# Performance work log

Hardware: AMD Instinct MI355X
Metric: run time of the kernel (lower is better)

The kernel has to match this reference:

```python
import jax, jax.numpy as jnp
import numpy as np

B, C, H, W = 8, 256, 48, 48
CK = 64  # C // k
WSCALE = 0.3 / np.sqrt(C)  # keep exp(QK^T) finite (original has no 1/sqrt(d) scaling)


def conv1x1(x, w, b):
    # x: (B,C,H,W), w: (O,C,1,1), b: (O,) -> (B,O,H,W)
    return jnp.einsum('bchw,oc->bohw', x, w[:, :, 0, 0]) + b[None, :, None, None]


def setup_inputs() -> dict:
    key = jax.random.key(0)
    ks = jax.random.split(key, 6)
    x = jax.random.normal(ks[0], (B, C, H, W), dtype=jnp.float32)
    qw = jax.random.normal(ks[1], (CK, C, 1, 1), dtype=jnp.float32) * WSCALE
    kw = jax.random.normal(ks[2], (CK, C, 1, 1), dtype=jnp.float32) * WSCALE
    vw = jax.random.normal(ks[3], (C, C, 1, 1), dtype=jnp.float32) * (1.0 / np.sqrt(C))
    gw = jax.random.normal(ks[4], (C, C, 1, 1), dtype=jnp.float32) * (1.0 / np.sqrt(C))
    zk = jnp.zeros((CK,), dtype=jnp.float32)
    zc = jnp.zeros((C,), dtype=jnp.float32)
    return {
        'x': x,
        'query_weight': qw, 'query_bias': zk,
        'key_weight': kw, 'key_bias': zk,
        'value_weight': vw, 'value_bias': zc,
        'gamma_weight': gw, 'gamma_bias': zc,
        'k': 4,
    }


def reference(x, query_weight, query_bias, key_weight, key_bias,
              value_weight, value_bias, gamma_weight, gamma_bias, k):
    b, c, h, w = x.shape
    n = h * w
    q = conv1x1(x, query_weight, query_bias).reshape(b, -1, n)   # (B,Ck,N)
    kk = conv1x1(x, key_weight, key_bias).reshape(b, -1, n)      # (B,Ck,N)
    # energy[b,i,j] = q_i . k_j  (queries on rows, no sqrt(d) scaling)
    energy = jnp.einsum('bci,bcj->bij', q, kk)                   # (B,N,N)
    energy = jnp.exp(energy)
    energy = energy / jnp.sum(energy, axis=2, keepdims=True)     # unnormalized-softmax over keys
    v = conv1x1(x, value_weight, value_bias).reshape(b, c, n)    # (B,C,N)
    # out[b,c,j] = sum_i v[b,c,i] * energy[b,i,j]  (faithful to torch.bmm(V, energy))
    out = jnp.einsum('bci,bij->bcj', v, energy).reshape(b, c, h, w)
    out = conv1x1(out, gamma_weight, gamma_bias)
    return out
```

## Files before the change

### kernel.cpp

```cpp
#include <hip/hip_runtime.h>

#define BATCH 8
#define CIN   256
#define NPIX  2304
#define CKD   64
#define NIT   (NPIX / 16)
#define NIC   (NPIX / 32)
#define NJB   (NPIX / 64)

typedef _Float16 f16;
typedef __attribute__((ext_vector_type(4))) _Float16 f16x4;
typedef __attribute__((ext_vector_type(8))) _Float16 f16x8;
typedef __attribute__((ext_vector_type(4))) float    f32x4;


__global__ __launch_bounds__(256) void cast_w(
    const float* __restrict__ qw, const float* __restrict__ kw,
    const float* __restrict__ vw, const float* __restrict__ gw,
    f16* __restrict__ Wqk, f16* __restrict__ Wv, f16* __restrict__ Wg)
{
    int idx = (blockIdx.x * 256 + threadIdx.x) * 4;
    const float* src;
    f16* dst;
    if (idx < 16384)      { src = qw + idx;           dst = Wqk + idx; }
    else if (idx < 32768) { src = kw + (idx - 16384); dst = Wqk + idx; }
    else if (idx < 98304) { src = vw + (idx - 32768); dst = Wv + (idx - 32768); }
    else                  { src = gw + (idx - 98304); dst = Wg + (idx - 98304); }
    float4 v = *(const float4*)src;
    f16x4 h = { (f16)v.x, (f16)v.y, (f16)v.z, (f16)v.w };
    *(f16x4*)dst = h;
}

__global__ __launch_bounds__(256) void cast_xT(
    const float* __restrict__ x, f16* __restrict__ xT)
{
    __shared__ float s[64][65];
    const int t = threadIdx.x;
    const int n0 = blockIdx.x * 64, c0 = blockIdx.y * 64, b = blockIdx.z;
    const float* xb = x + ((size_t)b * CIN + c0) * NPIX + n0;

    const int cl = t >> 4, ng = (t & 15) * 4;
    #pragma unroll
    for (int p = 0; p < 4; ++p) {
        float4 v = *(const float4*)(xb + (size_t)(cl + 16 * p) * NPIX + ng);
        s[cl + 16 * p][ng + 0] = v.x;
        s[cl + 16 * p][ng + 1] = v.y;
        s[cl + 16 * p][ng + 2] = v.z;
        s[cl + 16 * p][ng + 3] = v.w;
    }
    __syncthreads();
    const int nl = t >> 2, cs = (t & 3) * 16;
    f16 h[16];
    #pragma unroll
    for (int j = 0; j < 16; ++j) h[j] = (f16)s[cs + j][nl];
    f16* gp = &xT[((size_t)b * NPIX + n0 + nl) * CIN + c0 + cs];
    *(f16x8*)gp       = *(f16x8*)&h[0];
    *(f16x8*)(gp + 8) = *(f16x8*)&h[8];
}

__global__ __launch_bounds__(256) void qk_conv_mfma(
    const f16* __restrict__ xT, const f16* __restrict__ Wqk,
    const float* __restrict__ qbias, const float* __restrict__ kbias,
    f16* __restrict__ q_blk, f16* __restrict__ k_blk)
{
    __shared__ __align__(16) f16 us[32 * 136];
    const int t = threadIdx.x, w = t >> 6, lane = t & 63;
    const int quad = lane >> 4, l16 = lane & 15;
    const int wm = w & 1, wn = w >> 1;
    const int n0 = blockIdx.x * 32, b = blockIdx.y;

    const f16* bp = xT + ((size_t)b * NPIX + n0 + 16 * wn + l16) * CIN;
    const f16* ap = Wqk + (size_t)(64 * wm + l16) * CIN;

    f32x4 acc[4];
    #pragma unroll
    for (int mt = 0; mt < 4; ++mt) acc[mt] = (f32x4){0.f, 0.f, 0.f, 0.f};

    #pragma unroll
    for (int kk = 0; kk < CIN; kk += 32) {
        f16x8 bf = *(const f16x8*)(bp + kk + quad * 8);
        #pragma unroll
        for (int mt = 0; mt < 4; ++mt) {
            f16x8 af = *(const f16x8*)(ap + (size_t)mt * 16 * CIN + kk + quad * 8);
            acc[mt] = __builtin_amdgcn_mfma_f32_16x16x32_f16(af, bf, acc[mt], 0, 0, 0);
        }
    }
    const float* bias = wm ? kbias - 64 : qbias;
    #pragma unroll
    for (int mt = 0; mt < 4; ++mt) {
        int ob = 64 * wm + 16 * mt + quad * 4;
        #pragma unroll
        for (int r = 0; r < 4; ++r)
            us[(16 * wn + l16) * 136 + ob + r] = (f16)(acc[mt][r] + bias[ob + r]);
    }
    __syncthreads();
    {
        int ks2 = t >> 7, nt = (t >> 6) & 1, ln = t & 63;
        const f16* usr = &us[(nt * 16 + (ln & 15)) * 136 + ks2 * 32 + (ln >> 4) * 8];
        size_t base = (((size_t)b * NIT + (n0 >> 4) + nt) * 2 + ks2) * 512 + ln * 8;
        *(f16x8*)&q_blk[base] = *(const f16x8*)(usr);
        *(f16x8*)&k_blk[base] = *(const f16x8*)(usr + 64);
    }
}

#define ESL 136
__global__ __launch_bounds__(256) void energy_S(
    const f16* __restrict__ q_blk, const f16* __restrict__ k_blk,
    float* __restrict__ Pred)
{
    __shared__ __align__(16) f16 es[64 * ESL];
    __shared__ float red2[2][128];
    const int t    = threadIdx.x;
    const int w    = t >> 6, lane = t & 63;
    const int quad = lane >> 4, l16 = lane & 15;
    const int j0 = blockIdx.x * 64, i0 = blockIdx.y * 128, b = blockIdx.z;
    const size_t ln8 = (size_t)lane * 8;
    const f16* qb = q_blk + (size_t)b * NIT * 2 * 512 + ln8;

    f32x4 acc[8];
    #pragma unroll
    for (int mt = 0; mt < 8; ++mt) acc[mt] = (f32x4){0.f, 0.f, 0.f, 0.f};

    #pragma unroll
    for (int ks = 0; ks < 2; ++ks) {
        f16x8 bf = *(const f16x8*)(k_blk +
            (((size_t)b * NIT + (j0 >> 4) + w) * 2 + ks) * 512 + ln8);
        #pragma unroll
        for (int mt = 0; mt < 8; ++mt) {
            f16x8 af = *(const f16x8*)(qb + ((size_t)((i0 >> 4) + mt) * 2 + ks) * 512);
            acc[mt] = __builtin_amdgcn_mfma_f32_16x16x32_f16(af, bf, acc[mt], 0, 0, 0);
        }
    }

    #pragma unroll
    for (int mt = 0; mt < 8; ++mt) {
        f16x4 h = { (f16)__expf(acc[mt][0]), (f16)__expf(acc[mt][1]),
                    (f16)__expf(acc[mt][2]), (f16)__expf(acc[mt][3]) };
        *(f16x4*)&es[(16 * w + l16) * ESL + 16 * mt + quad * 4] = h;
    }
    __syncthreads();
    {
        int i = t & 127, jq = t >> 7;
        float s = 0.f;
        #pragma unroll
        for (int jj = 0; jj < 32; ++jj)
            s += (float)es[(jq * 32 + jj) * ESL + i];
        red2[jq][i] = s;
    }
    __syncthreads();
    if (t < 128)
        Pred[((size_t)blockIdx.x * BATCH + b) * NPIX + i0 + t] =
            red2[0][t] + red2[1][t];
}

__global__ __launch_bounds__(256) void reduce_S(
    const float* __restrict__ Pred, float* __restrict__ S)
{
    const size_t BN = (size_t)BATCH * NPIX;
    size_t idx = (size_t)blockIdx.x * 256 + threadIdx.x;
    float s = 0.f;
    #pragma unroll
    for (int jb = 0; jb < NJB; ++jb)
        s += Pred[(size_t)jb * BN + idx];
    S[idx] = s;
}

__global__ __launch_bounds__(256) void v_conv_mfma(
    const f16* __restrict__ xT, const f16* __restrict__ Wv,
    const float* __restrict__ vbias, const float* __restrict__ S,
    f16* __restrict__ u_blk)
{
    __shared__ __align__(16) f16 smem[9216];
    f16* As = smem;
    f16* Bs = smem + 128 * 40;
    f16* us = smem;
    const int t = threadIdx.x, w = t >> 6, lane = t & 63;
    const int quad = lane >> 4, l16 = lane & 15;
    const int wm = w & 1, wn = w >> 1;
    const int i0 = blockIdx.x * 64, c0 = blockIdx.y * 128, b = blockIdx.z;
    const int sub = t >> 2, le = t & 3;
    const f16* srcA = Wv + (size_t)(c0 + sub) * CIN + le * 8;
    const f16* srcB = xT + ((size_t)b * NPIX + i0 + sub) * CIN + le * 8;
    const int ldsw = sub * 40 + le * 8;

    f32x4 acc[4][2];
    #pragma unroll
    for (int mt = 0; mt < 4; ++mt)
        #pragma unroll
        for (int nt = 0; nt < 2; ++nt)
            acc[mt][nt] = (f32x4){0.f, 0.f, 0.f, 0.f};

    for (int kk = 0; kk < CIN; kk += 32) {
        f16x8 ta0 = *(const f16x8*)(srcA + kk);
        f16x8 ta1 = *(const f16x8*)(srcA + (size_t)64 * CIN + kk);
        f16x8 tb0 = *(const f16x8*)(srcB + kk);
        __syncthreads();
        *(f16x8*)&As[ldsw]           = ta0;
        *(f16x8*)&As[64 * 40 + ldsw] = ta1;
        *(f16x8*)&Bs[ldsw]           = tb0;
        __syncthreads();
        f16x8 af[4], bf[2];
        #pragma unroll
        for (int mt = 0; mt < 4; ++mt)
            af[mt] = *(const f16x8*)&As[(64 * wm + 16 * mt + l16) * 40 + quad * 8];
        #pragma unroll
        for (int nt = 0; nt < 2; ++nt)
            bf[nt] = *(const f16x8*)&Bs[(32 * wn + 16 * nt + l16) * 40 + quad * 8];
        #pragma unroll
        for (int mt = 0; mt < 4; ++mt)
            #pragma unroll
            for (int nt = 0; nt < 2; ++nt)
                acc[mt][nt] = __builtin_amdgcn_mfma_f32_16x16x32_f16(
                    af[mt], bf[nt], acc[mt][nt], 0, 0, 0);
    }

    __syncthreads();
    #pragma unroll
    for (int nt = 0; nt < 2; ++nt) {
        int i = 32 * wn + 16 * nt + l16;
        float is = 1.0f / S[(size_t)b * NPIX + i0 + i];
        #pragma unroll
        for (int mt = 0; mt < 4; ++mt)
            #pragma unroll
            for (int r = 0; r < 4; ++r) {
                int c = 64 * wm + 16 * mt + quad * 4 + r;
                us[c * 72 + i] = (f16)((acc[mt][nt][r] + vbias[c0 + c]) * is);
            }
    }
    __syncthreads();
    #pragma unroll
    for (int p = 0; p < 4; ++p) {
        int g  = t + 256 * p;
        int ct = g >> 7, ic = (g >> 6) & 1, ln = g & 63;
        f16x8 v = *(const f16x8*)&us[(ct * 16 + (ln & 15)) * 72 + ic * 32 + (ln >> 4) * 8];
        *(f16x8*)&u_blk[(((size_t)b * 16 + (c0 >> 4) + ct) * NIC + (i0 >> 5) + ic) * 512 + ln * 8] = v;
    }
}

__global__ __launch_bounds__(512, 4) void fused_bmm(
    const f16* __restrict__ q_blk, const f16* __restrict__ k_blk,
    const f16* __restrict__ u_blk, f16* __restrict__ o1T)
{
    __shared__ __align__(16) f16 es[2][8][512];
    const int t = threadIdx.x, w = t >> 6, lane = t & 63;
    const int quad = lane >> 4, l16 = lane & 15;
    const int bid = blockIdx.x;
    const int b  = bid & 7;
    const int j0 = (bid >> 3) * 64;
    const size_t ln8 = (size_t)lane * 8;

    const f16* qb = q_blk + (size_t)b * NIT * 2 * 512 + ln8;
    const f16* ub = u_blk + (size_t)b * 16 * NIC * 512 + ln8;

    const int iw = w >> 1;
    const int jh = w & 1;

    f16x8 kf[2][2];
    #pragma unroll
    for (int jj = 0; jj < 2; ++jj)
        #pragma unroll
        for (int ks = 0; ks < 2; ++ks)
            kf[jj][ks] = *(const f16x8*)(k_blk +
                (((size_t)b * NIT + (j0 >> 4) + jh + 2 * jj) * 2 + ks) * 512 + ln8);

    const int CT0 = w * 2;
    const int woff = ((iw & 1) * 2 + (quad >> 1)) * 128 + l16 * 8 + (quad & 1) * 4;
    const int et0 = jh * 2 + (iw >> 1);
    const int et1 = (jh + 2) * 2 + (iw >> 1);

    f32x4 acc[2][4];
    #pragma unroll
    for (int mt = 0; mt < 2; ++mt)
        #pragma unroll
        for (int jt = 0; jt < 4; ++jt)
            acc[mt][jt] = (f32x4){0.f, 0.f, 0.f, 0.f};

    for (int ic = 0; ic < NPIX / 64; ++ic) {
        const int cur = ic & 1;
        f32x4 e0 = (f32x4){0.f, 0.f, 0.f, 0.f};
        f32x4 e1 = (f32x4){0.f, 0.f, 0.f, 0.f};
        #pragma unroll
        for (int ks = 0; ks < 2; ++ks) {
            f16x8 af = *(const f16x8*)(qb + ((size_t)(ic * 4 + iw) * 2 + ks) * 512);
            e0 = __builtin_amdgcn_mfma_f32_16x16x32_f16(af, kf[0][ks], e0, 0, 0, 0);
            e1 = __builtin_amdgcn_mfma_f32_16x16x32_f16(af, kf[1][ks], e1, 0, 0, 0);
        }
        f16x4 h0 = { (f16)__expf(e0[0]), (f16)__expf(e0[1]),
                     (f16)__expf(e0[2]), (f16)__expf(e0[3]) };
        f16x4 h1 = { (f16)__expf(e1[0]), (f16)__expf(e1[1]),
                     (f16)__expf(e1[2]), (f16)__expf(e1[3]) };
        *(f16x4*)&es[cur][et0][woff] = h0;
        *(f16x4*)&es[cur][et1][woff] = h1;
        __syncthreads();
        #pragma unroll
        for (int isub = 0; isub < 2; ++isub) {
            f16x8 af0 = *(const f16x8*)(ub + ((size_t)(CT0 + 0) * NIC + ic * 2 + isub) * 512);
            f16x8 af1 = *(const f16x8*)(ub + ((size_t)(CT0 + 1) * NIC + ic * 2 + isub) * 512);
            #pragma unroll
            for (int jt = 0; jt < 4; ++jt) {
                f16x8 bf = *(const f16x8*)&es[cur][jt * 2 + isub][ln8];
                acc[0][jt] = __builtin_amdgcn_mfma_f32_16x16x32_f16(af0, bf, acc[0][jt], 0, 0, 0);
                acc[1][jt] = __builtin_amdgcn_mfma_f32_16x16x32_f16(af1, bf, acc[1][jt], 0, 0, 0);
            }
        }
    }

    #pragma unroll
    for (int mt = 0; mt < 2; ++mt) {
        int cb = 32 * w + 16 * mt + quad * 4;
        #pragma unroll
        for (int jt = 0; jt < 4; ++jt) {
            int j = j0 + 16 * jt + l16;
            f16x4 h2 = { (f16)acc[mt][jt][0], (f16)acc[mt][jt][1],
                         (f16)acc[mt][jt][2], (f16)acc[mt][jt][3] };
            *(f16x4*)&o1T[((size_t)b * NPIX + j) * CIN + cb] = h2;
        }
    }
}

__global__ __launch_bounds__(256) void gamma_conv_mfma(
    const f16* __restrict__ o1T, const f16* __restrict__ Wg,
    const float* __restrict__ gbias, float* __restrict__ out)
{
    __shared__ __align__(16) f16 As[128 * 40];
    __shared__ __align__(16) f16 Bs[64 * 40];
    const int t = threadIdx.x, w = t >> 6, lane = t & 63;
    const int quad = lane >> 4, l16 = lane & 15;
    const int wm = w & 1, wn = w >> 1;
    const int j0 = blockIdx.x * 64, o0 = blockIdx.y * 128, b = blockIdx.z;
    const int sub = t >> 2, le = t & 3;
    const f16* srcA = Wg + (size_t)(o0 + sub) * CIN + le * 8;
    const f16* srcB = o1T + ((size_t)b * NPIX + j0 + sub) * CIN + le * 8;
    const int ldsw = sub * 40 + le * 8;

    f32x4 acc[4][2];
    #pragma unroll
    for (int mt = 0; mt < 4; ++mt)
        #pragma unroll
        for (int nt = 0; nt < 2; ++nt)
            acc[mt][nt] = (f32x4){0.f, 0.f, 0.f, 0.f};

    for (int kk = 0; kk < CIN; kk += 32) {
        f16x8 ta0 = *(const f16x8*)(srcA + kk);
        f16x8 ta1 = *(const f16x8*)(srcA + (size_t)64 * CIN + kk);
        f16x8 tb0 = *(const f16x8*)(srcB + kk);
        __syncthreads();
        *(f16x8*)&As[ldsw]           = ta0;
        *(f16x8*)&As[64 * 40 + ldsw] = ta1;
        *(f16x8*)&Bs[ldsw]           = tb0;
        __syncthreads();
        f16x8 af[4], bf[2];
        #pragma unroll
        for (int mt = 0; mt < 4; ++mt)
            af[mt] = *(const f16x8*)&As[(64 * wm + 16 * mt + l16) * 40 + quad * 8];
        #pragma unroll
        for (int nt = 0; nt < 2; ++nt)
            bf[nt] = *(const f16x8*)&Bs[(32 * wn + 16 * nt + l16) * 40 + quad * 8];
        #pragma unroll
        for (int mt = 0; mt < 4; ++mt)
            #pragma unroll
            for (int nt = 0; nt < 2; ++nt)
                acc[mt][nt] = __builtin_amdgcn_mfma_f32_16x16x32_f16(
                    af[mt], bf[nt], acc[mt][nt], 0, 0, 0);
    }

    #pragma unroll
    for (int mt = 0; mt < 4; ++mt)
        #pragma unroll
        for (int r = 0; r < 4; ++r) {
            int o = o0 + 64 * wm + 16 * mt + quad * 4 + r;
            float bv = gbias[o];
            #pragma unroll
            for (int nt = 0; nt < 2; ++nt) {
                int j = j0 + 32 * wn + 16 * nt + l16;
                out[((size_t)b * CIN + o) * NPIX + j] = acc[mt][nt][r] + bv;
            }
        }
}

extern "C" void kernel_launch(void* const* d_in, const int* in_sizes, int n_in,
                              void* d_out, int out_size, void* d_ws, size_t ws_size,
                              hipStream_t stream) {
    const float* x   = (const float*)d_in[0];
    const float* qw  = (const float*)d_in[1];
    const float* qbv = (const float*)d_in[2];
    const float* kw  = (const float*)d_in[3];
    const float* kbv = (const float*)d_in[4];
    const float* vw  = (const float*)d_in[5];
    const float* vbv = (const float*)d_in[6];
    const float* gw  = (const float*)d_in[7];
    const float* gbv = (const float*)d_in[8];
    float* out = (float*)d_out;

    const size_t BCN  = (size_t)BATCH * CIN * NPIX;
    const size_t BN   = (size_t)BATCH * NPIX;
    const size_t BNCK = (size_t)BATCH * NPIX * CKD;

    f16* q_blk = (f16*)d_ws;
    f16* k_blk = q_blk + BNCK;
    f16* u_blk = k_blk + BNCK;
    f16* xT    = u_blk + BCN;
    f16* o1T   = xT + BCN;
    f16* Wqk   = o1T + BCN;
    f16* Wv    = Wqk + 128 * 256;
    f16* Wg    = Wv + 256 * 256;
    float* S   = (float*)(Wg + 256 * 256);
    float* Pred= S + BN;

    cast_w<<<160, 256, 0, stream>>>(qw, kw, vw, gw, Wqk, Wv, Wg);
    cast_xT<<<dim3(NPIX / 64, CIN / 64, BATCH), 256, 0, stream>>>(x, xT);
    qk_conv_mfma<<<dim3(NPIX / 32, BATCH), 256, 0, stream>>>(xT, Wqk, qbv, kbv, q_blk, k_blk);
    energy_S<<<dim3(NPIX / 64, NPIX / 128, BATCH), 256, 0, stream>>>(q_blk, k_blk, Pred);
    reduce_S<<<(int)(BN / 256), 256, 0, stream>>>(Pred, S);
    v_conv_mfma<<<dim3(NPIX / 64, CIN / 128, BATCH), 256, 0, stream>>>(xT, Wv, vbv, S, u_blk);
    fused_bmm<<<NJB * BATCH, 512, 0, stream>>>(q_blk, k_blk, u_blk, o1T);
    gamma_conv_mfma<<<dim3(NPIX / 64, CIN / 128, BATCH), 256, 0, stream>>>(o1T, Wg, gbv, out);
}
```

Before: 202.8 us.

## Software-pipeline attention loop: prefetch Q/V fragments and overlap exp stage with PV MFMA

Restructures the fused energy/PV loop into a two-stage software pipeline unrolled by two. Global loads of the Q and U fragments for upcoming chunks are issued ahead of use, and the next chunk's QK MFMA plus exp is computed while the current chunk's PV MFMAs run. The old syncthreads is replaced by an explicit lgkmcnt wait and s_barrier. This is meant to hide global-load latency and the barrier stall, at the cost of more live registers, which could reduce occupancy.

Result: faster. 192.0 us (-5.3%).

```diff
diff --git a/kernel.cpp b/kernel.cpp
--- a/kernel.cpp
+++ b/kernel.cpp
@@ -7,6 +7,7 @@
 #define NIT   (NPIX / 16)
 #define NIC   (NPIX / 32)
 #define NJB   (NPIX / 64)
+#define NCH   (NPIX / 64)
 
 typedef _Float16 f16;
 typedef __attribute__((ext_vector_type(4))) _Float16 f16x4;
@@ -275,35 +276,72 @@
         for (int jt = 0; jt < 4; ++jt)
             acc[mt][jt] = (f32x4){0.f, 0.f, 0.f, 0.f};
 
-    for (int ic = 0; ic < NPIX / 64; ++ic) {
-        const int cur = ic & 1;
-        f32x4 e0 = (f32x4){0.f, 0.f, 0.f, 0.f};
-        f32x4 e1 = (f32x4){0.f, 0.f, 0.f, 0.f};
-        #pragma unroll
-        for (int ks = 0; ks < 2; ++ks) {
-            f16x8 af = *(const f16x8*)(qb + ((size_t)(ic * 4 + iw) * 2 + ks) * 512);
-            e0 = __builtin_amdgcn_mfma_f32_16x16x32_f16(af, kf[0][ks], e0, 0, 0, 0);
-            e1 = __builtin_amdgcn_mfma_f32_16x16x32_f16(af, kf[1][ks], e1, 0, 0, 0);
-        }
-        f16x4 h0 = { (f16)__expf(e0[0]), (f16)__expf(e0[1]),
-                     (f16)__expf(e0[2]), (f16)__expf(e0[3]) };
-        f16x4 h1 = { (f16)__expf(e1[0]), (f16)__expf(e1[1]),
-                     (f16)__expf(e1[2]), (f16)__expf(e1[3]) };
-        *(f16x4*)&es[cur][et0][woff] = h0;
-        *(f16x4*)&es[cur][et1][woff] = h1;
-        __syncthreads();
-        #pragma unroll
-        for (int isub = 0; isub < 2; ++isub) {
-            f16x8 af0 = *(const f16x8*)(ub + ((size_t)(CT0 + 0) * NIC + ic * 2 + isub) * 512);
-            f16x8 af1 = *(const f16x8*)(ub + ((size_t)(CT0 + 1) * NIC + ic * 2 + isub) * 512);
-            #pragma unroll
-            for (int jt = 0; jt < 4; ++jt) {
-                f16x8 bf = *(const f16x8*)&es[cur][jt * 2 + isub][ln8];
-                acc[0][jt] = __builtin_amdgcn_mfma_f32_16x16x32_f16(af0, bf, acc[0][jt], 0, 0, 0);
-                acc[1][jt] = __builtin_amdgcn_mfma_f32_16x16x32_f16(af1, bf, acc[1][jt], 0, 0, 0);
-            }
-        }
-    }
+#define QLD(ic, ks)  (*(const f16x8*)(qb + ((size_t)((ic) * 4 + iw) * 2 + (ks)) * 512))
+#define ULD(ct, ic, is) (*(const f16x8*)(ub + ((size_t)(CT0 + (ct)) * NIC + (ic) * 2 + (is)) * 512))
+
+#define STAGE1(q0, q1, buf) do {                                              \
+    f32x4 e0 = (f32x4){0.f, 0.f, 0.f, 0.f};                                   \
+    f32x4 e1 = (f32x4){0.f, 0.f, 0.f, 0.f};                                   \
+    e0 = __builtin_amdgcn_mfma_f32_16x16x32_f16(q0, kf[0][0], e0, 0, 0, 0);   \
+    e0 = __builtin_amdgcn_mfma_f32_16x16x32_f16(q1, kf[0][1], e0, 0, 0, 0);   \
+    e1 = __builtin_amdgcn_mfma_f32_16x16x32_f16(q0, kf[1][0], e1, 0, 0, 0);   \
+    e1 = __builtin_amdgcn_mfma_f32_16x16x32_f16(q1, kf[1][1], e1, 0, 0, 0);   \
+    f16x4 h0 = { (f16)__expf(e0[0]), (f16)__expf(e0[1]),                      \
+                 (f16)__expf(e0[2]), (f16)__expf(e0[3]) };                    \
+    f16x4 h1 = { (f16)__expf(e1[0]), (f16)__expf(e1[1]),                      \
+                 (f16)__expf(e1[2]), (f16)__expf(e1[3]) };                    \
+    *(f16x4*)&es[buf][et0][woff] = h0;                                        \
+    *(f16x4*)&es[buf][et1][woff] = h1;                                        \
+} while (0)
+
+#define STAGE2(buf, u00, u01, u10, u11) do {                                  \
+    _Pragma("unroll")                                                         \
+    for (int jt = 0; jt < 4; ++jt) {                                          \
+        f16x8 bf0 = *(const f16x8*)&es[buf][jt * 2 + 0][ln8];                 \
+        acc[0][jt] = __builtin_amdgcn_mfma_f32_16x16x32_f16(u00, bf0, acc[0][jt], 0, 0, 0); \
+        acc[1][jt] = __builtin_amdgcn_mfma_f32_16x16x32_f16(u10, bf0, acc[1][jt], 0, 0, 0); \
+        f16x8 bf1 = *(const f16x8*)&es[buf][jt * 2 + 1][ln8];                 \
+        acc[0][jt] = __builtin_amdgcn_mfma_f32_16x16x32_f16(u01, bf1, acc[0][jt], 0, 0, 0); \
+        acc[1][jt] = __builtin_amdgcn_mfma_f32_16x16x32_f16(u11, bf1, acc[1][jt], 0, 0, 0); \
+    }                                                                         \
+} while (0)
+
+#define BAR() do {                                                            \
+    asm volatile("s_waitcnt lgkmcnt(0)" ::: "memory");                        \
+    __builtin_amdgcn_s_barrier();                                             \
+} while (0)
+
+    f16x8 qA0 = QLD(0, 0), qA1 = QLD(0, 1);
+    f16x8 uA0 = ULD(0, 0, 0), uA1 = ULD(0, 0, 1);
+    f16x8 uA2 = ULD(1, 0, 0), uA3 = ULD(1, 0, 1);
+    f16x8 qB0 = QLD(1, 0), qB1 = QLD(1, 1);
+    STAGE1(qA0, qA1, 0);
+    BAR();
+
+    f16x8 uB0, uB1, uB2, uB3;
+    for (int ic = 0; ic < NCH; ic += 2) {
+        const int i1 = ic + 1;
+        const int i2 = (ic + 2 < NCH) ? ic + 2 : NCH - 1;
+        const int i3 = (ic + 3 < NCH) ? ic + 3 : NCH - 1;
+        uB0 = ULD(0, i1, 0); uB1 = ULD(0, i1, 1);
+        uB2 = ULD(1, i1, 0); uB3 = ULD(1, i1, 1);
+        qA0 = QLD(i2, 0); qA1 = QLD(i2, 1);
+        STAGE2(0, uA0, uA1, uA2, uA3);
+        STAGE1(qB0, qB1, 1);
+        BAR();
+        uA0 = ULD(0, i2, 0); uA1 = ULD(0, i2, 1);
+        uA2 = ULD(1, i2, 0); uA3 = ULD(1, i2, 1);
+        qB0 = QLD(i3, 0); qB1 = QLD(i3, 1);
+        STAGE2(1, uB0, uB1, uB2, uB3);
+        if (ic + 2 < NCH) STAGE1(qA0, qA1, 0);
+        BAR();
+    }
+
+#undef QLD
+#undef ULD
+#undef STAGE1
+#undef STAGE2
+#undef BAR
 
     #pragma unroll
     for (int mt = 0; mt < 2; ++mt) {
```

## Split fused_bmm over pixel quarters with full-LDS exp tiles and sum partials in gamma conv

Applied to the files above, without the earlier changes.

Splits the attention-V product into four pixel-range partial blocks per output tile, quadrupling the grid. Each block first computes all of its exp(QK) tiles into a large dynamic LDS buffer, then runs a sync-free MFMA loop with double-buffered register prefetch of V. The gamma conv reads and sums the four fp16 partial outputs, reusing the xT buffer for one of them. This trades more LDS use, lower occupancy, extra partial-output traffic and fp16 partial rounding for more parallelism and fewer barriers.

Result: faster. 190.8 us (-5.9%).

```diff
diff --git a/kernel.cpp b/kernel.cpp
--- a/kernel.cpp
+++ b/kernel.cpp
@@ -7,6 +7,9 @@
 #define NIT   (NPIX / 16)
 #define NIC   (NPIX / 32)
 #define NJB   (NPIX / 64)
+#define NQ    4
+#define ICQ   (NIC / NQ)
+#define IT16Q (NIT / NQ)
 
 typedef _Float16 f16;
 typedef __attribute__((ext_vector_type(4))) _Float16 f16x4;
@@ -239,21 +242,27 @@
 
 __global__ __launch_bounds__(512, 4) void fused_bmm(
     const f16* __restrict__ q_blk, const f16* __restrict__ k_blk,
-    const f16* __restrict__ u_blk, f16* __restrict__ o1T)
-{
-    __shared__ __align__(16) f16 es[2][8][512];
+    const f16* __restrict__ u_blk,
+    f16* __restrict__ o1A, f16* __restrict__ o1B,
+    f16* __restrict__ o1C, f16* __restrict__ o1D)
+{
+    extern __shared__ __align__(16) f16 es[];
     const int t = threadIdx.x, w = t >> 6, lane = t & 63;
     const int quad = lane >> 4, l16 = lane & 15;
     const int bid = blockIdx.x;
-    const int b  = bid & 7;
-    const int j0 = (bid >> 3) * 64;
+    const int b   = bid & 7;
+    const int r   = bid >> 3;
+    const int q   = r & 3;
+    const int jb  = r >> 2;
+    const int j0  = jb * 64;
+    f16* __restrict__ o1h = (q == 0) ? o1A : (q == 1) ? o1B : (q == 2) ? o1C : o1D;
     const size_t ln8 = (size_t)lane * 8;
 
     const f16* qb = q_blk + (size_t)b * NIT * 2 * 512 + ln8;
     const f16* ub = u_blk + (size_t)b * 16 * NIC * 512 + ln8;
 
-    const int iw = w >> 1;
-    const int jh = w & 1;
+    const int iw0 = w >> 1;
+    const int jh  = w & 1;
 
     f16x8 kf[2][2];
     #pragma unroll
@@ -264,46 +273,57 @@
                 (((size_t)b * NIT + (j0 >> 4) + jh + 2 * jj) * 2 + ks) * 512 + ln8);
 
     const int CT0 = w * 2;
-    const int woff = ((iw & 1) * 2 + (quad >> 1)) * 128 + l16 * 8 + (quad & 1) * 4;
-    const int et0 = jh * 2 + (iw >> 1);
-    const int et1 = (jh + 2) * 2 + (iw >> 1);
-
-    f32x4 acc[2][4];
-    #pragma unroll
-    for (int mt = 0; mt < 2; ++mt)
-        #pragma unroll
-        for (int jt = 0; jt < 4; ++jt)
-            acc[mt][jt] = (f32x4){0.f, 0.f, 0.f, 0.f};
-
-    for (int ic = 0; ic < NPIX / 64; ++ic) {
-        const int cur = ic & 1;
+
+    #pragma unroll
+    for (int s = 0; s < 9; ++s) {
+        const int i16 = iw0 + 4 * s;
+        const int gi  = q * IT16Q + i16;
+        f16x8 q0 = *(const f16x8*)(qb + ((size_t)gi * 2 + 0) * 512);
+        f16x8 q1 = *(const f16x8*)(qb + ((size_t)gi * 2 + 1) * 512);
         f32x4 e0 = (f32x4){0.f, 0.f, 0.f, 0.f};
         f32x4 e1 = (f32x4){0.f, 0.f, 0.f, 0.f};
-        #pragma unroll
-        for (int ks = 0; ks < 2; ++ks) {
-            f16x8 af = *(const f16x8*)(qb + ((size_t)(ic * 4 + iw) * 2 + ks) * 512);
-            e0 = __builtin_amdgcn_mfma_f32_16x16x32_f16(af, kf[0][ks], e0, 0, 0, 0);
-            e1 = __builtin_amdgcn_mfma_f32_16x16x32_f16(af, kf[1][ks], e1, 0, 0, 0);
-        }
+        e0 = __builtin_amdgcn_mfma_f32_16x16x32_f16(q0, kf[0][0], e0, 0, 0, 0);
+        e0 = __builtin_amdgcn_mfma_f32_16x16x32_f16(q1, kf[0][1], e0, 0, 0, 0);
+        e1 = __builtin_amdgcn_mfma_f32_16x16x32_f16(q0, kf[1][0], e1, 0, 0, 0);
+        e1 = __builtin_amdgcn_mfma_f32_16x16x32_f16(q1, kf[1][1], e1, 0, 0, 0);
         f16x4 h0 = { (f16)__expf(e0[0]), (f16)__expf(e0[1]),
                      (f16)__expf(e0[2]), (f16)__expf(e0[3]) };
         f16x4 h1 = { (f16)__expf(e1[0]), (f16)__expf(e1[1]),
                      (f16)__expf(e1[2]), (f16)__expf(e1[3]) };
-        *(f16x4*)&es[cur][et0][woff] = h0;
-        *(f16x4*)&es[cur][et1][woff] = h1;
-        __syncthreads();
-        #pragma unroll
-        for (int isub = 0; isub < 2; ++isub) {
-            f16x8 af0 = *(const f16x8*)(ub + ((size_t)(CT0 + 0) * NIC + ic * 2 + isub) * 512);
-            f16x8 af1 = *(const f16x8*)(ub + ((size_t)(CT0 + 1) * NIC + ic * 2 + isub) * 512);
-            #pragma unroll
-            for (int jt = 0; jt < 4; ++jt) {
-                f16x8 bf = *(const f16x8*)&es[cur][jt * 2 + isub][ln8];
-                acc[0][jt] = __builtin_amdgcn_mfma_f32_16x16x32_f16(af0, bf, acc[0][jt], 0, 0, 0);
-                acc[1][jt] = __builtin_amdgcn_mfma_f32_16x16x32_f16(af1, bf, acc[1][jt], 0, 0, 0);
-            }
+        const int woff = ((i16 & 1) * 2 + (quad >> 1)) * 128 + l16 * 8 + (quad & 1) * 4;
+        const int tb   = (i16 >> 1) * 4;
+        *(f16x4*)&es[(size_t)(tb + jh) * 512 + woff]     = h0;
+        *(f16x4*)&es[(size_t)(tb + jh + 2) * 512 + woff] = h1;
+    }
+
+    const int g0 = q * ICQ;
+#define ULD(ct, icg) (*(const f16x8*)(ub + ((size_t)(CT0 + (ct)) * NIC + (icg)) * 512))
+    f16x8 ua = ULD(0, g0),     ub2 = ULD(1, g0);
+    f16x8 na = ULD(0, g0 + 1), nb  = ULD(1, g0 + 1);
+    asm volatile("s_waitcnt lgkmcnt(0)" ::: "memory");
+    __builtin_amdgcn_s_barrier();
+
+    f32x4 acc[2][4];
+    #pragma unroll
+    for (int mt = 0; mt < 2; ++mt)
+        #pragma unroll
+        for (int jt = 0; jt < 4; ++jt)
+            acc[mt][jt] = (f32x4){0.f, 0.f, 0.f, 0.f};
+
+    __builtin_amdgcn_s_setprio(1);
+    for (int ic2 = 0; ic2 < ICQ; ++ic2) {
+        f16x8 fa, fb2;
+        if (ic2 + 2 < ICQ) { fa = ULD(0, g0 + ic2 + 2); fb2 = ULD(1, g0 + ic2 + 2); }
+        #pragma unroll
+        for (int jt = 0; jt < 4; ++jt) {
+            f16x8 bf = *(const f16x8*)&es[(size_t)(ic2 * 4 + jt) * 512 + ln8];
+            acc[0][jt] = __builtin_amdgcn_mfma_f32_16x16x32_f16(ua,  bf, acc[0][jt], 0, 0, 0);
+            acc[1][jt] = __builtin_amdgcn_mfma_f32_16x16x32_f16(ub2, bf, acc[1][jt], 0, 0, 0);
         }
-    }
+        ua = na; ub2 = nb; na = fa; nb = fb2;
+    }
+    __builtin_amdgcn_s_setprio(0);
+#undef ULD
 
     #pragma unroll
     for (int mt = 0; mt < 2; ++mt) {
@@ -313,13 +333,15 @@
             int j = j0 + 16 * jt + l16;
             f16x4 h2 = { (f16)acc[mt][jt][0], (f16)acc[mt][jt][1],
                          (f16)acc[mt][jt][2], (f16)acc[mt][jt][3] };
-            *(f16x4*)&o1T[((size_t)b * NPIX + j) * CIN + cb] = h2;
+            *(f16x4*)&o1h[((size_t)b * NPIX + j) * CIN + cb] = h2;
         }
     }
 }
 
 __global__ __launch_bounds__(256) void gamma_conv_mfma(
-    const f16* __restrict__ o1T, const f16* __restrict__ Wg,
+    const f16* __restrict__ o1A, const f16* __restrict__ o1B,
+    const f16* __restrict__ o1C, const f16* __restrict__ o1D,
+    const f16* __restrict__ Wg,
     const float* __restrict__ gbias, float* __restrict__ out)
 {
     __shared__ __align__(16) f16 As[128 * 40];
@@ -329,8 +351,8 @@
     const int wm = w & 1, wn = w >> 1;
     const int j0 = blockIdx.x * 64, o0 = blockIdx.y * 128, b = blockIdx.z;
     const int sub = t >> 2, le = t & 3;
-    const f16* srcA = Wg + (size_t)(o0 + sub) * CIN + le * 8;
-    const f16* srcB = o1T + ((size_t)b * NPIX + j0 + sub) * CIN + le * 8;
+    const f16* srcA  = Wg + (size_t)(o0 + sub) * CIN + le * 8;
+    const size_t boff = ((size_t)b * NPIX + j0 + sub) * CIN + le * 8;
     const int ldsw = sub * 40 + le * 8;
 
     f32x4 acc[4][2];
@@ -343,7 +365,15 @@
     for (int kk = 0; kk < CIN; kk += 32) {
         f16x8 ta0 = *(const f16x8*)(srcA + kk);
         f16x8 ta1 = *(const f16x8*)(srcA + (size_t)64 * CIN + kk);
-        f16x8 tb0 = *(const f16x8*)(srcB + kk);
+        f16x8 t0 = *(const f16x8*)(o1A + boff + kk);
+        f16x8 t1 = *(const f16x8*)(o1B + boff + kk);
+        f16x8 t2 = *(const f16x8*)(o1C + boff + kk);
+        f16x8 t3 = *(const f16x8*)(o1D + boff + kk);
+        f16x8 tb0;
+        #pragma unroll
+        for (int e = 0; e < 8; ++e)
+            tb0[e] = (f16)(((float)t0[e] + (float)t1[e]) +
+                           ((float)t2[e] + (float)t3[e]));
         __syncthreads();
         *(f16x8*)&As[ldsw]           = ta0;
         *(f16x8*)&As[64 * 40 + ldsw] = ta1;
@@ -406,6 +436,8 @@
     f16* Wg    = Wv + 256 * 256;
     float* S   = (float*)(Wg + 256 * 256);
     float* Pred= S + BN;
+    f16* o1C   = (f16*)(Pred + (size_t)NJB * BN);
+    f16* o1D   = o1C + BCN;
 
     cast_w<<<160, 256, 0, stream>>>(qw, kw, vw, gw, Wqk, Wv, Wg);
     cast_xT<<<dim3(NPIX / 64, CIN / 64, BATCH), 256, 0, stream>>>(x, xT);
@@ -413,6 +445,8 @@
     energy_S<<<dim3(NPIX / 64, NPIX / 128, BATCH), 256, 0, stream>>>(q_blk, k_blk, Pred);
     reduce_S<<<(int)(BN / 256), 256, 0, stream>>>(Pred, S);
     v_conv_mfma<<<dim3(NPIX / 64, CIN / 128, BATCH), 256, 0, stream>>>(xT, Wv, vbv, S, u_blk);
-    fused_bmm<<<NJB * BATCH, 512, 0, stream>>>(q_blk, k_blk, u_blk, o1T);
-    gamma_conv_mfma<<<dim3(NPIX / 64, CIN / 128, BATCH), 256, 0, stream>>>(o1T, Wg, gbv, out);
-}
+    fused_bmm<<<NJB * NQ * BATCH, 512, 72 * 1024, stream>>>(
+        q_blk, k_blk, u_blk, o1T, xT, o1C, o1D);
+    gamma_conv_mfma<<<dim3(NPIX / 64, CIN / 128, BATCH), 256, 0, stream>>>(
+        o1T, xT, o1C, o1D, Wg, gbv, out);
+}
```
